# Kernel optimization log

Measured on AMD Instinct MI355X. Metric: run time of the kernel, lower is better.

## Reference

```python
import jax, jax.numpy as jnp
import numpy as np

B, L, F = 4, 8192, 1024
H, D = 16, 64
EPS = 1e-6

def _phi(x):
    # ELU+1 positive feature map, standard for linear attention
    return jax.nn.elu(x) + 1.0

def setup_inputs() -> dict:
    key = jax.random.key(0)
    ks = jax.random.split(key, 6)
    s_in = 1.0
    s_w = 1.0 / np.sqrt(F)
    s_o = 1.0 / np.sqrt(H * D)
    return {
        "inputs_q": jax.random.normal(ks[0], (B, L, F), jnp.float32),
        "inputs_kv": jax.random.normal(ks[1], (B, L, F), jnp.float32),
        "Wq": jax.random.normal(ks[2], (F, H, D), jnp.float32) * s_w,
        "Wk": jax.random.normal(ks[3], (F, H, D), jnp.float32) * s_w,
        "Wv": jax.random.normal(ks[4], (F, H, D), jnp.float32) * s_w,
        "Wo": jax.random.normal(ks[5], (H, D, F), jnp.float32) * s_o,
    }

def reference(inputs_q, inputs_kv, Wq, Wk, Wv, Wo):
    # QKV projections (split-head kernels, no bias)
    q = jnp.einsum('bqf,fhd->bqhd', inputs_q, Wq)   # [B,Lq,H,D]
    k = jnp.einsum('bkf,fhd->bkhd', inputs_kv, Wk)  # [B,Lk,H,D]
    v = jnp.einsum('bkf,fhd->bkhd', inputs_kv, Wv)  # [B,Lk,H,D]

    qp = _phi(q)
    kp = _phi(k)

    # Linear attention: O = phi(q) @ (phi(k)^T V) / (phi(q) . sum_k phi(k))
    kv = jnp.einsum('bkhd,bkhe->bhde', kp, v)       # [B,H,D,D] small state
    ksum = jnp.sum(kp, axis=1)                       # [B,H,D]
    z = 1.0 / (jnp.einsum('bqhd,bhd->bqh', qp, ksum) + EPS)
    out = jnp.einsum('bqhd,bhde,bqh->bqhe', qp, kv, z)  # [B,Lq,H,D]

    # Output projection
    return jnp.einsum('bqhe,hef->bqf', out, Wo)      # [B,Lq,F]
```

## Files before the change

kernel.cpp:

```cpp
#include <hip/hip_runtime.h>
#include <hip/hip_fp16.h>
#include <math.h>

typedef _Float16 half8  __attribute__((ext_vector_type(8)));
typedef _Float16 half4v __attribute__((ext_vector_type(4)));
typedef float    floatx4 __attribute__((ext_vector_type(4)));

#define NB   4
#define LL   8192
#define FF   1024
#define HH   16
#define DD   64
#define MTOT 32768
#define KK   1024
#define NN   1024
#define ZSCALE 65536.0f

__device__ __forceinline__ void gload_lds16(const void* g, void* l) {
  __builtin_amdgcn_global_load_lds(
      (const __attribute__((address_space(1))) void*)g,
      (__attribute__((address_space(3))) void*)l, 16, 0, 0);
}

__device__ __forceinline__ float phi_act(float x) {
  return x > 0.f ? x + 1.f : __expf(x);
}

__global__ void k_cvt(const float* __restrict__ src, _Float16* __restrict__ dst, int n4) {
  int stride = gridDim.x * blockDim.x;
  for (int i = blockIdx.x * blockDim.x + threadIdx.x; i < n4; i += stride) {
    float4 v = reinterpret_cast<const float4*>(src)[i];
    half4v h;
    h[0] = (_Float16)v.x; h[1] = (_Float16)v.y; h[2] = (_Float16)v.z; h[3] = (_Float16)v.w;
    reinterpret_cast<half4v*>(dst)[i] = h;
  }
}

__global__ void k_cvt_t(const float* __restrict__ W0, const float* __restrict__ W1,
                        const float* __restrict__ W2,
                        _Float16* __restrict__ T0, _Float16* __restrict__ T1,
                        _Float16* __restrict__ T2) {
  __shared__ float tile[32][33];
  int bid = blockIdx.x;
  int w = bid >> 10, rem = bid & 1023;
  int ti = rem >> 5, tj = rem & 31;
  const float* src = (w == 0) ? W0 : (w == 1) ? W1 : W2;
  _Float16*    dst = (w == 0) ? T0 : (w == 1) ? T1 : T2;
  int t = threadIdx.x;
  int r = t >> 3, c4 = (t & 7) << 2;
  float4 v = *reinterpret_cast<const float4*>(&src[(size_t)(ti * 32 + r) * FF + tj * 32 + c4]);
  tile[r][c4 + 0] = v.x; tile[r][c4 + 1] = v.y; tile[r][c4 + 2] = v.z; tile[r][c4 + 3] = v.w;
  __syncthreads();
  half4v h;
  h[0] = (_Float16)tile[c4 + 0][r];
  h[1] = (_Float16)tile[c4 + 1][r];
  h[2] = (_Float16)tile[c4 + 2][r];
  h[3] = (_Float16)tile[c4 + 3][r];
  *reinterpret_cast<half4v*>(&dst[(size_t)(tj * 32 + r) * FF + ti * 32 + c4]) = h;
}


__device__ __forceinline__ void stage_plane(const _Float16* __restrict__ G, int row0,
                                            int col0, _Float16* plane, int tid) {
  #pragma unroll
  for (int is = 0; is < 2; ++is) {
    int lin = is * 8192 + tid * 16;
    int swz = lin ^ (((lin >> 7) & 3) << 4);
    int row = swz >> 6, kcb = swz & 63;
    gload_lds16(G + (size_t)(row0 + row) * 1024 + col0 + (kcb >> 1),
                (char*)plane + lin);
  }
}

template<int BUF, int KKH, int MH, bool LOADB>
__device__ __forceinline__ void do_phase(const _Float16* smem, floatx4 (&acc)[8][4],
                                         half8 (&bfr)[4], int wr, int wc, int lr, int khix) {
  asm volatile("s_waitcnt vmcnt(6)" ::: "memory");
  __builtin_amdgcn_sched_barrier(0);
  __builtin_amdgcn_s_barrier();
  __builtin_amdgcn_sched_barrier(0);
  const _Float16* pa = smem + (BUF * 2 + KKH) * 8192 + (wr * 128 + MH * 64 + lr) * 32 + khix * 8;
  const _Float16* pb = smem + 32768 + (BUF * 2 + KKH) * 8192 + (wc * 64 + lr) * 32 + khix * 8;
  half8 af[4];
  #pragma unroll
  for (int mm = 0; mm < 4; ++mm) af[mm] = *(const half8*)(pa + mm * 16 * 32);
  if constexpr (LOADB) {
    #pragma unroll
    for (int n = 0; n < 4; ++n) bfr[n] = *(const half8*)(pb + n * 16 * 32);
  }
  __builtin_amdgcn_s_setprio(1);
  #pragma unroll
  for (int mm = 0; mm < 4; ++mm)
    #pragma unroll
    for (int n = 0; n < 4; ++n)
      acc[MH * 4 + mm][n] =
          __builtin_amdgcn_mfma_f32_16x16x32_f16(af[mm], bfr[n], acc[MH * 4 + mm][n], 0, 0, 0);
  __builtin_amdgcn_s_setprio(0);
}

template<int MODE, bool PHI>
__global__ __launch_bounds__(512, 2)
void k_gemm(const _Float16* __restrict__ A, const _Float16* __restrict__ BT,
            void* __restrict__ Cptr, float outScale) {
  __shared__ __align__(16) _Float16 smem[65536];
  const int tid  = threadIdx.x;
  const int lane = tid & 63;
  const int wid  = tid >> 6;
  const int wr = wid >> 2, wc = wid & 3;
  const int lr = lane & 15, lh = lane >> 4;
  const int khix = lh ^ ((lr >> 1) & 3);

  const int tile = (blockIdx.x & 7) * 64 + (blockIdx.x >> 3);
  const int tm = tile >> 2, tn = tile & 3;
  const int i0 = tm * 256, j0 = tn * 256;

  const _Float16* Ab = A;
  const _Float16* Bb = (MODE == 2) ? BT + ((size_t)(i0 >> 13)) * ((size_t)NN * KK) : BT;

  floatx4 acc[8][4];
  #pragma unroll
  for (int m = 0; m < 8; ++m)
    #pragma unroll
    for (int n = 0; n < 4; ++n)
      #pragma unroll
      for (int r = 0; r < 4; ++r) acc[m][n][r] = 0.f;

  _Float16* sm = (_Float16*)smem;
  stage_plane(Ab, i0, 0,  sm + 0,             tid);
  stage_plane(Bb, j0, 0,  sm + 32768,         tid);
  stage_plane(Ab, i0, 32, sm + 8192,          tid);
  stage_plane(Bb, j0, 32, sm + 32768 + 8192,  tid);

  half8 bfr[4];
  #pragma unroll 1
  for (int t2 = 0; t2 < 8; ++t2) {
    const int ka = ((t2 * 2 + 1) & 15) * 64;
    const int kb = ((t2 * 2 + 2) & 15) * 64;
    stage_plane(Ab, i0, ka +  0, sm + 16384,                 tid);
    do_phase<0,0,0,true >(sm, acc, bfr, wr, wc, lr, khix);
    stage_plane(Bb, j0, ka +  0, sm + 32768 + 16384,         tid);
    do_phase<0,0,1,false>(sm, acc, bfr, wr, wc, lr, khix);
    stage_plane(Ab, i0, ka + 32, sm + 16384 + 8192,          tid);
    do_phase<0,1,0,true >(sm, acc, bfr, wr, wc, lr, khix);
    stage_plane(Bb, j0, ka + 32, sm + 32768 + 16384 + 8192,  tid);
    do_phase<0,1,1,false>(sm, acc, bfr, wr, wc, lr, khix);
    stage_plane(Ab, i0, kb +  0, sm + 0,                     tid);
    do_phase<1,0,0,true >(sm, acc, bfr, wr, wc, lr, khix);
    stage_plane(Bb, j0, kb +  0, sm + 32768,                 tid);
    do_phase<1,0,1,false>(sm, acc, bfr, wr, wc, lr, khix);
    stage_plane(Ab, i0, kb + 32, sm + 8192,                  tid);
    do_phase<1,1,0,true >(sm, acc, bfr, wr, wc, lr, khix);
    stage_plane(Bb, j0, kb + 32, sm + 32768 + 8192,          tid);
    do_phase<1,1,1,false>(sm, acc, bfr, wr, wc, lr, khix);
  }

  asm volatile("s_waitcnt vmcnt(0)" ::: "memory");
  __builtin_amdgcn_sched_barrier(0);
  __builtin_amdgcn_s_barrier();

  if constexpr (MODE == 0) {
    _Float16* C = (_Float16*)Cptr;
    #pragma unroll
    for (int m = 0; m < 8; ++m) {
      int row = i0 + wr * 128 + m * 16 + lh * 4;
      #pragma unroll
      for (int n = 0; n < 4; ++n) {
        int col = j0 + wc * 64 + n * 16 + lr;
        #pragma unroll
        for (int r = 0; r < 4; ++r) {
          float v = acc[m][n][r];
          if constexpr (PHI) v = phi_act(v);
          C[(size_t)(row + r) * NN + col] = (_Float16)v;
        }
      }
    }
  } else if constexpr (MODE == 2) {
    float* C = (float*)Cptr;
    #pragma unroll
    for (int m = 0; m < 8; ++m) {
      int row = i0 + wr * 128 + m * 16 + lh * 4;
      #pragma unroll
      for (int n = 0; n < 4; ++n) {
        int col = j0 + wc * 64 + n * 16 + lr;
        #pragma unroll
        for (int r = 0; r < 4; ++r)
          C[(size_t)(row + r) * NN + col] = acc[m][n][r] * outScale;
      }
    }
  } else {
    #pragma unroll
    for (int m = 0; m < 8; ++m) {
      int l0l = wr * 128 + m * 16 + lh * 4;
      #pragma unroll
      for (int n = 0; n < 4; ++n) {
        int n_loc = wc * 64 + n * 16 + lr;
        int byte = (n_loc * 512 + l0l * 2) ^ ((n_loc & 7) << 4);
        half4v h;
        #pragma unroll
        for (int r = 0; r < 4; ++r) {
          float v = acc[m][n][r];
          if constexpr (PHI) v = phi_act(v);
          h[r] = (_Float16)v;
        }
        *(half4v*)((char*)sm + byte) = h;
      }
    }
    __syncthreads();
    _Float16* C = (_Float16*)Cptr;
    const int bb = i0 >> 13;
    const int l0 = i0 & 8191;
    #pragma unroll 1
    for (int pass = 0; pass < 16; ++pass) {
      int n_loc = pass * 16 + (tid >> 5);
      int lo = (tid & 31) * 16;
      int byte = (n_loc * 512 + lo) ^ ((n_loc & 7) << 4);
      half8 v = *(const half8*)((char*)sm + byte);
      *(half8*)&C[((size_t)bb * 1024 + j0 + n_loc) * LL + l0 + (lo >> 1)] = v;
    }
  }
}

__global__ void k_ksum(const _Float16* __restrict__ kpT, float* __restrict__ ksum) {
  int w = threadIdx.x >> 6, lane = threadIdx.x & 63;
  int row = blockIdx.x * 4 + w;
  const _Float16* p = kpT + (size_t)row * LL;
  float s = 0.f;
  for (int j = 0; j < 16; ++j) {
    half8 v = *(const half8*)&p[j * 512 + lane * 8];
    #pragma unroll
    for (int e = 0; e < 8; ++e) s += (float)v[e];
  }
  #pragma unroll
  for (int off = 1; off < 64; off <<= 1) s += __shfl_xor(s, off);
  if (lane == 0) ksum[row] = s;
}

__global__ __launch_bounds__(64)
void k_stageB(const _Float16* __restrict__ kpT, const _Float16* __restrict__ vT,
              float* __restrict__ kvpart) {
  __shared__ _Float16 Ak[64 * 72];
  __shared__ _Float16 Bv[64 * 72];
  const int bid = blockIdx.x;
  const int bh = bid >> 4, cc = bid & 15;
  const int lane = threadIdx.x;
  const int lr = lane & 15, lh = lane >> 4;
  const _Float16* Ab = kpT + (size_t)bh * 64 * LL + cc * 512;
  const _Float16* Bb = vT  + (size_t)bh * 64 * LL + cc * 512;

  floatx4 acc[4][4];
  #pragma unroll
  for (int m = 0; m < 4; ++m)
    #pragma unroll
    for (int n = 0; n < 4; ++n)
      #pragma unroll
      for (int r = 0; r < 4; ++r) acc[m][n][r] = 0.f;

  for (int kt = 0; kt < 512; kt += 64) {
    __syncthreads();
    #pragma unroll
    for (int j = 0; j < 8; ++j) {
      int chunk = lane + 64 * j;
      int rr = chunk >> 3;
      int off = (chunk & 7) * 8;
      *(half8*)&Ak[rr * 72 + off] = *(const half8*)&Ab[(size_t)rr * LL + kt + off];
      *(half8*)&Bv[rr * 72 + off] = *(const half8*)&Bb[(size_t)rr * LL + kt + off];
    }
    __syncthreads();
    #pragma unroll
    for (int ks = 0; ks < 2; ++ks) {
      half8 af[4], bf[4];
      #pragma unroll
      for (int m = 0; m < 4; ++m) af[m] = *(const half8*)&Ak[(m * 16 + lr) * 72 + ks * 32 + lh * 8];
      #pragma unroll
      for (int n = 0; n < 4; ++n) bf[n] = *(const half8*)&Bv[(n * 16 + lr) * 72 + ks * 32 + lh * 8];
      #pragma unroll
      for (int m = 0; m < 4; ++m)
        #pragma unroll
        for (int n = 0; n < 4; ++n)
          acc[m][n] = __builtin_amdgcn_mfma_f32_16x16x32_f16(af[m], bf[n], acc[m][n], 0, 0, 0);
    }
  }
  float* op = kvpart + (size_t)bid * 4096;
  #pragma unroll
  for (int m = 0; m < 4; ++m)
    #pragma unroll
    for (int n = 0; n < 4; ++n)
      #pragma unroll
      for (int r = 0; r < 4; ++r)
        op[(m * 16 + lh * 4 + r) * 64 + n * 16 + lr] = acc[m][n][r];
}

__global__ void k_reduce_kv(const float* __restrict__ kvpart, float* __restrict__ kv) {
  int gid = blockIdx.x * 256 + threadIdx.x;
  int bh = gid >> 12, i = gid & 4095;
  float s = 0.f;
  for (int c = 0; c < 16; ++c) s += kvpart[((size_t)bh * 16 + c) * 4096 + i];
  kv[gid] = s;
}

__global__ void k_zscale(_Float16* __restrict__ qp, const float* __restrict__ ksum) {
  int w = threadIdx.x >> 6, lane = threadIdx.x & 63;
  int row = blockIdx.x * 4 + w;
  int b = row >> 13;
  int h = lane >> 2;
  _Float16* p = qp + (size_t)row * 1024 + lane * 16;
  half8 v0 = *(half8*)&p[0];
  half8 v1 = *(half8*)&p[8];
  const float* ks = ksum + ((size_t)b * 16 + h) * 64 + (lane & 3) * 16;
  float dot = 0.f;
  #pragma unroll
  for (int e = 0; e < 8; ++e) dot += (float)v0[e] * ks[e];
  #pragma unroll
  for (int e = 0; e < 8; ++e) dot += (float)v1[e] * ks[8 + e];
  dot += __shfl_xor(dot, 1);
  dot += __shfl_xor(dot, 2);
  float zf = ZSCALE / (dot + 1e-6f);
  #pragma unroll
  for (int e = 0; e < 8; ++e) v0[e] = (_Float16)((float)v0[e] * zf);
  #pragma unroll
  for (int e = 0; e < 8; ++e) v1[e] = (_Float16)((float)v1[e] * zf);
  *(half8*)&p[0] = v0;
  *(half8*)&p[8] = v1;
}

__global__ __launch_bounds__(256)
void k_mker(const float* __restrict__ kv, const _Float16* __restrict__ Wo16,
            _Float16* __restrict__ MT) {
  __shared__ float kvs[4096];
  int bid = blockIdx.x;
  int fc = bid & 3, h = (bid >> 2) & 15, b = bid >> 6;
  const float* kvp = kv + ((size_t)b * 16 + h) * 4096;
  for (int i = threadIdx.x; i < 4096; i += 256) kvs[i] = kvp[i];
  __syncthreads();
  int f = fc * 256 + threadIdx.x;
  float acc[64];
  #pragma unroll
  for (int d = 0; d < 64; ++d) acc[d] = 0.f;
  for (int e = 0; e < 64; ++e) {
    float wv = (float)Wo16[(size_t)(h * 64 + e) * 1024 + f];
    #pragma unroll
    for (int d = 0; d < 64; ++d) acc[d] = fmaf(kvs[d * 64 + e], wv, acc[d]);
  }
  _Float16* op = MT + ((size_t)b * 1024 + f) * 1024 + h * 64;
  #pragma unroll
  for (int g = 0; g < 8; ++g) {
    half8 o;
    #pragma unroll
    for (int j = 0; j < 8; ++j) o[j] = (_Float16)acc[g * 8 + j];
    *(half8*)&op[g * 8] = o;
  }
}

extern "C" void kernel_launch(void* const* d_in, const int* in_sizes, int n_in,
                              void* d_out, int out_size, void* d_ws, size_t ws_size,
                              hipStream_t stream) {
  (void)in_sizes; (void)n_in; (void)out_size; (void)ws_size;
  const float* xq  = (const float*)d_in[0];
  const float* xkv = (const float*)d_in[1];
  const float* Wq  = (const float*)d_in[2];
  const float* Wk  = (const float*)d_in[3];
  const float* Wv  = (const float*)d_in[4];
  const float* Wo  = (const float*)d_in[5];

  char* ws = (char*)d_ws;
  _Float16* qp16 = (_Float16*)(ws + 0);
  _Float16* kpT  = (_Float16*)(ws + 67108864);
  _Float16* vT   = (_Float16*)(ws + 134217728);
  _Float16* WqT  = (_Float16*)(ws + 201326592);
  _Float16* WkT  = (_Float16*)(ws + 203423744);
  _Float16* WvT  = (_Float16*)(ws + 205520896);
  _Float16* Wo16 = (_Float16*)(ws + 207618048);
  float*    ksum = (float*)(ws + 209715200);
  float*    kv   = (float*)(ws + 209731584);
  float*    kvpart = (float*)(ws + 210780160);
  _Float16* MT   = (_Float16*)(ws + 227557376);

  _Float16* Xq16  = (_Float16*)d_out;
  _Float16* Xkv16 = Xq16 + 33554432;

  k_cvt<<<2048, 256, 0, stream>>>(xq,  Xq16,  8388608);
  k_cvt<<<2048, 256, 0, stream>>>(xkv, Xkv16, 8388608);
  k_cvt<<<512,  256, 0, stream>>>(Wo,  Wo16,  262144);
  k_cvt_t<<<3072, 256, 0, stream>>>(Wq, Wk, Wv, WqT, WkT, WvT);

  k_gemm<0, true ><<<512, 512, 0, stream>>>(Xq16,  WqT, qp16, 1.0f);
  k_gemm<1, true ><<<512, 512, 0, stream>>>(Xkv16, WkT, kpT,  1.0f);
  k_gemm<1, false><<<512, 512, 0, stream>>>(Xkv16, WvT, vT,   1.0f);

  k_ksum<<<1024, 256, 0, stream>>>(kpT, ksum);
  k_stageB<<<1024, 64, 0, stream>>>(kpT, vT, kvpart);
  k_reduce_kv<<<1024, 256, 0, stream>>>(kvpart, kv);

  k_zscale<<<8192, 256, 0, stream>>>(qp16, ksum);

  k_mker<<<256, 256, 0, stream>>>(kv, Wo16, MT);
  k_gemm<2, false><<<512, 512, 0, stream>>>(qp16, MT, d_out, 1.0f / ZSCALE);
}
```

Before: 520.0 us.

## Reorder GEMM pipeline: issue LDS fragment reads before barrier, relax vmcnt waits

Moves the per-phase global-to-LDS staging into do_phase and issues the LDS fragment reads for the current plane before the workgroup barrier instead of after it. The vmcnt wait now happens only on every other phase and allows 4 outstanding loads, and a full vmcnt(0) plus barrier is added after the prologue. The goal is to overlap LDS reads with barrier latency and cut synchronization stalls in the main K loop. Correctness now depends on the relaxed wait counts still guaranteeing that each plane has landed before it is read, which is a subtle ordering risk.

```diff
diff --git a/kernel.cpp b/kernel.cpp
--- a/kernel.cpp
+++ b/kernel.cpp
@@ -72,22 +72,28 @@
   }
 }
 
-template<int BUF, int KKH, int MH, bool LOADB>
-__device__ __forceinline__ void do_phase(const _Float16* smem, floatx4 (&acc)[8][4],
+template<int BUF, int KKH, int MH, bool LOADB, bool VM4>
+__device__ __forceinline__ void do_phase(const _Float16* __restrict__ Gst, int srow0, int scol0,
+                                         _Float16* splane, int tid,
+                                         const _Float16* sm, floatx4 (&acc)[8][4],
                                          half8 (&bfr)[4], int wr, int wc, int lr, int khix) {
-  asm volatile("s_waitcnt vmcnt(6)" ::: "memory");
+  stage_plane(Gst, srow0, scol0, splane, tid);
+  const _Float16* pa = sm + (BUF * 2 + KKH) * 8192 + (wr * 128 + MH * 64 + lr) * 32 + khix * 8;
+  const _Float16* pb = sm + 32768 + (BUF * 2 + KKH) * 8192 + (wc * 64 + lr) * 32 + khix * 8;
+  half8 af[4];
+  #pragma unroll
+  for (int mm = 0; mm < 4; ++mm) af[mm] = *(const half8*)(pa + mm * 16 * 32);
+  if constexpr (LOADB) {
+    #pragma unroll
+    for (int n = 0; n < 4; ++n) bfr[n] = *(const half8*)(pb + n * 16 * 32);
+  }
   __builtin_amdgcn_sched_barrier(0);
+  if constexpr (VM4) {
+    asm volatile("s_waitcnt vmcnt(4)" ::: "memory");
+    __builtin_amdgcn_sched_barrier(0);
+  }
   __builtin_amdgcn_s_barrier();
   __builtin_amdgcn_sched_barrier(0);
-  const _Float16* pa = smem + (BUF * 2 + KKH) * 8192 + (wr * 128 + MH * 64 + lr) * 32 + khix * 8;
-  const _Float16* pb = smem + 32768 + (BUF * 2 + KKH) * 8192 + (wc * 64 + lr) * 32 + khix * 8;
-  half8 af[4];
-  #pragma unroll
-  for (int mm = 0; mm < 4; ++mm) af[mm] = *(const half8*)(pa + mm * 16 * 32);
-  if constexpr (LOADB) {
-    #pragma unroll
-    for (int n = 0; n < 4; ++n) bfr[n] = *(const half8*)(pb + n * 16 * 32);
-  }
   __builtin_amdgcn_s_setprio(1);
   #pragma unroll
   for (int mm = 0; mm < 4; ++mm)
@@ -130,28 +136,24 @@
   stage_plane(Bb, j0, 0,  sm + 32768,         tid);
   stage_plane(Ab, i0, 32, sm + 8192,          tid);
   stage_plane(Bb, j0, 32, sm + 32768 + 8192,  tid);
+  asm volatile("s_waitcnt vmcnt(0)" ::: "memory");
+  __builtin_amdgcn_sched_barrier(0);
+  __builtin_amdgcn_s_barrier();
+  __builtin_amdgcn_sched_barrier(0);
 
   half8 bfr[4];
   #pragma unroll 1
   for (int t2 = 0; t2 < 8; ++t2) {
     const int ka = ((t2 * 2 + 1) & 15) * 64;
     const int kb = ((t2 * 2 + 2) & 15) * 64;
-    stage_plane(Ab, i0, ka +  0, sm + 16384,                 tid);
-    do_phase<0,0,0,true >(sm, acc, bfr, wr, wc, lr, khix);
-    stage_plane(Bb, j0, ka +  0, sm + 32768 + 16384,         tid);
-    do_phase<0,0,1,false>(sm, acc, bfr, wr, wc, lr, khix);
-    stage_plane(Ab, i0, ka + 32, sm + 16384 + 8192,          tid);
-    do_phase<0,1,0,true >(sm, acc, bfr, wr, wc, lr, khix);
-    stage_plane(Bb, j0, ka + 32, sm + 32768 + 16384 + 8192,  tid);
-    do_phase<0,1,1,false>(sm, acc, bfr, wr, wc, lr, khix);
-    stage_plane(Ab, i0, kb +  0, sm + 0,                     tid);
-    do_phase<1,0,0,true >(sm, acc, bfr, wr, wc, lr, khix);
-    stage_plane(Bb, j0, kb +  0, sm + 32768,                 tid);
-    do_phase<1,0,1,false>(sm, acc, bfr, wr, wc, lr, khix);
-    stage_plane(Ab, i0, kb + 32, sm + 8192,                  tid);
-    do_phase<1,1,0,true >(sm, acc, bfr, wr, wc, lr, khix);
-    stage_plane(Bb, j0, kb + 32, sm + 32768 + 8192,          tid);
-    do_phase<1,1,1,false>(sm, acc, bfr, wr, wc, lr, khix);
+    do_phase<0,0,0,true ,false>(Ab, i0, ka +  0, sm + 16384,                tid, sm, acc, bfr, wr, wc, lr, khix);
+    do_phase<0,0,1,false,true >(Bb, j0, ka +  0, sm + 32768 + 16384,        tid, sm, acc, bfr, wr, wc, lr, khix);
+    do_phase<0,1,0,true ,false>(Ab, i0, ka + 32, sm + 16384 + 8192,         tid, sm, acc, bfr, wr, wc, lr, khix);
+    do_phase<0,1,1,false,true >(Bb, j0, ka + 32, sm + 32768 + 16384 + 8192, tid, sm, acc, bfr, wr, wc, lr, khix);
+    do_phase<1,0,0,true ,false>(Ab, i0, kb +  0, sm + 0,                    tid, sm, acc, bfr, wr, wc, lr, khix);
+    do_phase<1,0,1,false,true >(Bb, j0, kb +  0, sm + 32768,                tid, sm, acc, bfr, wr, wc, lr, khix);
+    do_phase<1,1,0,true ,false>(Ab, i0, kb + 32, sm + 8192,                 tid, sm, acc, bfr, wr, wc, lr, khix);
+    do_phase<1,1,1,false,true >(Bb, j0, kb + 32, sm + 32768 + 8192,         tid, sm, acc, bfr, wr, wc, lr, khix);
   }
 
   asm volatile("s_waitcnt vmcnt(0)" ::: "memory");
```

After: 513.0 us. About the same (-1.4%).
